# Kernel optimization log

Measured on AMD Instinct MI355X. Metric: run time of the kernel, lower is better.

Reference implementation:

```python
import jax, jax.numpy as jnp
import numpy as np

B, T, C = 16, 2048, 64  # n_embd = 64


def setup_inputs() -> dict:
    key = jax.random.key(0)
    ks = jax.random.split(key, 4)
    scale = 1.0 / np.sqrt(C)
    x = jax.random.normal(ks[0], (B, T, C), dtype=jnp.float32)
    Wk = jax.random.normal(ks[1], (C, C), dtype=jnp.float32) * scale
    Wq = jax.random.normal(ks[2], (C, C), dtype=jnp.float32) * scale
    Wv = jax.random.normal(ks[3], (C, C), dtype=jnp.float32) * scale
    bk = jnp.zeros((C,), dtype=jnp.float32)
    bq = jnp.zeros((C,), dtype=jnp.float32)
    bv = jnp.zeros((C,), dtype=jnp.float32)
    return {"x": x, "Wk": Wk, "bk": bk, "Wq": Wq, "bq": bq, "Wv": Wv, "bv": bv}


def reference(x, Wk, bk, Wq, bq, Wv, bv):
    # Faithful to source: wei = q @ k^T * C**0.5 (MULTIPLY, as in original code),
    # softmax over last axis, no causal mask (tril is built but unused), dropout=0.
    _, _, c = x.shape
    k = jnp.einsum('btc,cd->btd', x, Wk) + bk
    q = jnp.einsum('btc,cd->btd', x, Wq) + bq
    v = jnp.einsum('btc,cd->btd', x, Wv) + bv
    wei = jnp.einsum('btd,bsd->bts', q, k) * (c ** 0.5)  # [B,T,T]
    wei = jax.nn.softmax(wei, axis=-1)
    out = jnp.einsum('bts,bsd->btd', wei, v)  # [B,T,C]
    return out
```

## Files before the change

### kernel.cpp

```cpp
#include <hip/hip_runtime.h>
#include <hip/hip_bf16.h>
#include <stdint.h>

#define NBATCH 16
#define NT 2048
#define NC 64
#define QT 128
#define KT 128
#define SC_LOG2E 11.5415603f

typedef __bf16 bf16x8 __attribute__((ext_vector_type(8)));
typedef float f32x4 __attribute__((ext_vector_type(4)));
typedef float f32x16 __attribute__((ext_vector_type(16)));

#define Z16 {0.f,0.f,0.f,0.f,0.f,0.f,0.f,0.f,0.f,0.f,0.f,0.f,0.f,0.f,0.f,0.f}

extern "C" __device__ float __ocml_exp2_f32(float);

static __device__ __forceinline__ unsigned short f2bf(float f) {
  __bf16 h = (__bf16)f;
  union { __bf16 h; unsigned short u; } a; a.h = h; return a.u;
}
static __device__ __forceinline__ float bf2f(unsigned short h) {
  union { uint32_t u; float f; } a; a.u = ((uint32_t)h) << 16;
  return a.f;
}
static __device__ __forceinline__ float fasu(uint32_t u) {
  union { uint32_t u; float f; } a; a.u = u; return a.f;
}
static __device__ __forceinline__ uint32_t uasf(float f) {
  union { float f; uint32_t u; } a; a.f = f; return a.u;
}

#define GLD_LDS16(gsrc, ldst)                                                  \
  __builtin_amdgcn_global_load_lds(                                            \
      (const __attribute__((address_space(1))) void*)(gsrc),                   \
      (__attribute__((address_space(3))) void*)(ldst), 16, 0, 0)

__global__ __launch_bounds__(256, 2) void prep_w(
    const float* __restrict__ Wk, const float* __restrict__ Wq,
    const float* __restrict__ Wv,
    unsigned short* __restrict__ wt_hi, unsigned short* __restrict__ wt_lo)
{
  __shared__ unsigned short hbuf[64][66];
  __shared__ unsigned short lbuf[64][66];
  const int m = (int)blockIdx.x;
  const float* Wm = (m == 0) ? Wk : (m == 1 ? Wq : Wv);
  const int tid = (int)threadIdx.x;
  for (int idx = tid; idx < 1024; idx += 256) {
    int c = idx >> 4, o4 = (idx & 15) * 4;
    float4 v = *(const float4*)(Wm + c * 64 + o4);
    float vals[4] = {v.x, v.y, v.z, v.w};
#pragma unroll
    for (int j = 0; j < 4; ++j) {
      unsigned short h = f2bf(vals[j]);
      hbuf[o4 + j][c] = h;
      lbuf[o4 + j][c] = f2bf(vals[j] - bf2f(h));
    }
  }
  __syncthreads();
  for (int idx = tid; idx < 1024; idx += 256) {
    int o = idx >> 4, c0 = (idx & 15) * 4;
    ushort4 hv, lv;
    hv.x = hbuf[o][c0]; hv.y = hbuf[o][c0 + 1];
    hv.z = hbuf[o][c0 + 2]; hv.w = hbuf[o][c0 + 3];
    lv.x = lbuf[o][c0]; lv.y = lbuf[o][c0 + 1];
    lv.z = lbuf[o][c0 + 2]; lv.w = lbuf[o][c0 + 3];
    *(ushort4*)(wt_hi + (size_t)(m * 64 + o) * 64 + c0) = hv;
    *(ushort4*)(wt_lo + (size_t)(m * 64 + o) * 64 + c0) = lv;
  }
}

__global__ __launch_bounds__(256, 2) void proj_kernel(
    const float* __restrict__ x,
    const unsigned short* __restrict__ wt_hi, const unsigned short* __restrict__ wt_lo,
    const float* __restrict__ bk, const float* __restrict__ bq, const float* __restrict__ bv,
    unsigned short* __restrict__ khi, unsigned short* __restrict__ klo,
    unsigned short* __restrict__ qhi, unsigned short* __restrict__ qlo,
    unsigned short* __restrict__ vt)
{
  __shared__ __align__(16) char smem[65536];
  const int XH = 0, XL = 8192, WTH = 16384, WTL = 40960, VTB = 0;
  const int tid = (int)threadIdx.x;
  const int l = tid & 63, w = tid >> 6;
  const int lr = l & 15, lg = l >> 4;
  const int blk = (int)blockIdx.x;
  const int rowbase = blk * 64;
  const int bb = blk >> 5;

  float4 xv[4];
#pragma unroll
  for (int j = 0; j < 4; ++j) {
    int c = tid + j * 256;
    int row = c >> 4, d0 = (c & 15) * 4;
    xv[j] = *(const float4*)(x + (size_t)(rowbase + row) * NC + d0);
  }
#pragma unroll
  for (int ch4 = 0; ch4 < 6; ++ch4) {
    int ch = ch4 * 4 + w;
    int d = ch * 1024 + l * 16;
    int swk = d ^ (((d >> 7) & 7) << 4);
    GLD_LDS16((const char*)wt_hi + swk, smem + WTH + ch * 1024);
    GLD_LDS16((const char*)wt_lo + swk, smem + WTL + ch * 1024);
  }
#pragma unroll
  for (int j = 0; j < 4; ++j) {
    int c = tid + j * 256;
    int row = c >> 4, d0 = (c & 15) * 4;
    unsigned short h0 = f2bf(xv[j].x), h1 = f2bf(xv[j].y), h2 = f2bf(xv[j].z), h3 = f2bf(xv[j].w);
    unsigned short m0 = f2bf(xv[j].x - bf2f(h0)), m1 = f2bf(xv[j].y - bf2f(h1));
    unsigned short m2 = f2bf(xv[j].z - bf2f(h2)), m3 = f2bf(xv[j].w - bf2f(h3));
    uint2 ph, pl;
    ph.x = (uint32_t)h0 | ((uint32_t)h1 << 16); ph.y = (uint32_t)h2 | ((uint32_t)h3 << 16);
    pl.x = (uint32_t)m0 | ((uint32_t)m1 << 16); pl.y = (uint32_t)m2 | ((uint32_t)m3 << 16);
    int byteoff = (row * 128 + d0 * 2) ^ ((row & 7) << 4);
    *(uint2*)(smem + XH + byteoff) = ph;
    *(uint2*)(smem + XL + byteoff) = pl;
  }
  __syncthreads();

  bf16x8 xh[2], xl[2];
  {
    int row = w * 16 + lr;
#pragma unroll
    for (int dc = 0; dc < 2; ++dc) {
      int byteoff = (row * 128 + (dc * 32 + lg * 8) * 2) ^ ((row & 7) << 4);
      xh[dc] = *(const bf16x8*)(smem + XH + byteoff);
      xl[dc] = *(const bf16x8*)(smem + XL + byteoff);
    }
  }
  f32x4 acc[12];
#pragma unroll
  for (int nb = 0; nb < 12; ++nb) {
    f32x4 a = {0.f, 0.f, 0.f, 0.f};
    int og = nb * 16 + lr;
#pragma unroll
    for (int dc = 0; dc < 2; ++dc) {
      int byteoff = (og * 128 + (dc * 32 + lg * 8) * 2) ^ ((og & 7) << 4);
      bf16x8 bh = *(const bf16x8*)(smem + WTH + byteoff);
      bf16x8 bl = *(const bf16x8*)(smem + WTL + byteoff);
      a = __builtin_amdgcn_mfma_f32_16x16x32_bf16(bh, xh[dc], a, 0, 0, 0);
      a = __builtin_amdgcn_mfma_f32_16x16x32_bf16(bl, xh[dc], a, 0, 0, 0);
      a = __builtin_amdgcn_mfma_f32_16x16x32_bf16(bh, xl[dc], a, 0, 0, 0);
    }
    acc[nb] = a;
  }
  __syncthreads();

  const int tloc = w * 16 + lr;
  const size_t gt = (size_t)(rowbase + tloc);
#pragma unroll
  for (int nb = 0; nb < 12; ++nb) {
    int ogb = (nb & 3) * 16 + lg * 4;
    const float* bp = (nb < 4) ? bk : (nb < 8 ? bq : bv);
    float4 bias = *(const float4*)(bp + ogb);
    float v0 = acc[nb][0] + bias.x, v1 = acc[nb][1] + bias.y,
          v2 = acc[nb][2] + bias.z, v3 = acc[nb][3] + bias.w;
    if (nb < 8) {
      if (nb >= 4) { v0 *= SC_LOG2E; v1 *= SC_LOG2E; v2 *= SC_LOG2E; v3 *= SC_LOG2E; }
      ushort4 hv, lv;
      hv.x = f2bf(v0); lv.x = f2bf(v0 - bf2f(hv.x));
      hv.y = f2bf(v1); lv.y = f2bf(v1 - bf2f(hv.y));
      hv.z = f2bf(v2); lv.z = f2bf(v2 - bf2f(hv.z));
      hv.w = f2bf(v3); lv.w = f2bf(v3 - bf2f(hv.w));
      unsigned short* dH = (nb < 4) ? khi : qhi;
      unsigned short* dL = (nb < 4) ? klo : qlo;
      *(ushort4*)(dH + gt * 64 + ogb) = hv;
      *(ushort4*)(dL + gt * 64 + ogb) = lv;
    } else {
      float vs[4] = {v0, v1, v2, v3};
#pragma unroll
      for (int r = 0; r < 4; ++r) {
        int o = ogb + r;
        int byteoff = (o * 128 + tloc * 2) ^ ((o & 7) << 4);
        *(unsigned short*)(smem + VTB + byteoff) = f2bf(vs[r]);
      }
    }
  }
  __syncthreads();
  for (int cc = tid; cc < 512; cc += 256) {
    int o = cc >> 3, t0 = (cc & 7) * 8;
    int byteoff = (o * 128 + t0 * 2) ^ ((o & 7) << 4);
    uint4 v = *(const uint4*)(smem + VTB + byteoff);
    *(uint4*)(vt + ((size_t)bb * 64 + o) * NT + (size_t)(blk & 31) * 64 + t0) = v;
  }
}

__global__ __launch_bounds__(512, 2) void attn_kernel(
    const unsigned short* __restrict__ khi, const unsigned short* __restrict__ klo,
    const unsigned short* __restrict__ qhi, const unsigned short* __restrict__ qlo,
    const unsigned short* __restrict__ vt,
    float* __restrict__ out)
{
  __shared__ __align__(16) char smem[98304];
  const int BUF = 49152;
  const int MLB = 65536;
  const int tid = (int)threadIdx.x;
  const int l = tid & 63, w = tid >> 6;
  const int lq = l & 31;
  const bool hi = (l >= 32);
  const int hioff = hi ? 16 : 0;
  const int r = w & 3;
  const int cc = w >> 2;
  const int lb = ((int)(blockIdx.x & 7) << 5) | ((int)blockIdx.x >> 3);
  const int bb = lb >> 4;
  const int qt = lb & 15;

  const char* kh_base = (const char*)(khi + (size_t)bb * NT * 64);
  const char* kl_base = (const char*)(klo + (size_t)bb * NT * 64);
  const char* v_base  = (const char*)(vt + (size_t)bb * 64 * NT);

#define STAGE_TILE(bufp_, it_)                                                 \
  do {                                                                         \
    const char* kh_t = kh_base + (size_t)(it_) * 16384;                        \
    const char* kl_t = kl_base + (size_t)(it_) * 16384;                        \
    const char* v_tb = v_base + (size_t)(it_) * 256;                           \
    _Pragma("unroll")                                                          \
    for (int j = 0; j < 2; ++j) {                                              \
      int ch = 2 * w + j;                                                      \
      int d = ch * 1024 + l * 16;                                              \
      int swk = d ^ (((d >> 7) & 7) << 4);                                     \
      GLD_LDS16(kh_t + swk, (bufp_) + ch * 1024);                              \
      GLD_LDS16(kl_t + swk, (bufp_) + 16384 + ch * 1024);                      \
      int o = d >> 8;                                                          \
      int swv = (d ^ ((o & 7) << 4)) & 255;                                    \
      GLD_LDS16(v_tb + (size_t)o * 4096 + swv, (bufp_) + 32768 + ch * 1024);   \
    }                                                                          \
  } while (0)

  STAGE_TILE(smem, 0);
  bf16x8 Qh[4], Ql[4];
  {
    const char* qh_t = (const char*)qhi + ((size_t)bb * NT + (size_t)qt * QT) * 128;
    const char* ql_t = (const char*)qlo + ((size_t)bb * NT + (size_t)qt * QT) * 128;
    int qrow = r * 32 + lq;
#pragma unroll
    for (int dc = 0; dc < 4; ++dc) {
      Qh[dc] = *(const bf16x8*)(qh_t + qrow * 128 + dc * 32 + hioff);
      Ql[dc] = *(const bf16x8*)(ql_t + qrow * 128 + dc * 32 + hioff);
    }
  }
  asm volatile("s_waitcnt vmcnt(0)" ::: "memory");
  __builtin_amdgcn_s_barrier();
  asm volatile("" ::: "memory");

  f32x16 O0 = Z16, O1 = Z16;
  float mrun = -1e30f, lrun = 0.f;
  const int swr = (lq & 7) << 4;

  for (int it = 0; it < NT / KT; ++it) {
    char* cb = smem + (it & 1) * BUF;
    if (it + 1 < NT / KT) STAGE_TILE(smem + ((it + 1) & 1) * BUF, it + 1);

    f32x16 T1a = Z16, T2a = Z16, T3a = Z16;
    f32x16 T1b = Z16, T2b = Z16, T3b = Z16;
    __builtin_amdgcn_s_setprio(1);
    {
      int row0 = cc * 64 + lq;
      int row1 = row0 + 32;
#pragma unroll
      for (int dc = 0; dc < 4; ++dc) {
        int cchunk = (dc * 32 + hioff) ^ swr;
        bf16x8 Ah0 = *(const bf16x8*)(cb + row0 * 128 + cchunk);
        bf16x8 Al0 = *(const bf16x8*)(cb + 16384 + row0 * 128 + cchunk);
        bf16x8 Ah1 = *(const bf16x8*)(cb + row1 * 128 + cchunk);
        bf16x8 Al1 = *(const bf16x8*)(cb + 16384 + row1 * 128 + cchunk);
        T1a = __builtin_amdgcn_mfma_f32_32x32x16_bf16(Ah0, Qh[dc], T1a, 0, 0, 0);
        T1b = __builtin_amdgcn_mfma_f32_32x32x16_bf16(Ah1, Qh[dc], T1b, 0, 0, 0);
        T2a = __builtin_amdgcn_mfma_f32_32x32x16_bf16(Al0, Qh[dc], T2a, 0, 0, 0);
        T2b = __builtin_amdgcn_mfma_f32_32x32x16_bf16(Al1, Qh[dc], T2b, 0, 0, 0);
        T3a = __builtin_amdgcn_mfma_f32_32x32x16_bf16(Ah0, Ql[dc], T3a, 0, 0, 0);
        T3b = __builtin_amdgcn_mfma_f32_32x32x16_bf16(Ah1, Ql[dc], T3b, 0, 0, 0);
      }
    }
    __builtin_amdgcn_s_setprio(0);
    f32x16 S0 = (T1a + T2a) + T3a;
    f32x16 S1 = (T1b + T2b) + T3b;

    float m01 = fmaxf(S0[0], S0[1]),   m23 = fmaxf(S0[2], S0[3]);
    float m45 = fmaxf(S0[4], S0[5]),   m67 = fmaxf(S0[6], S0[7]);
    float m89 = fmaxf(S0[8], S0[9]),   mab = fmaxf(S0[10], S0[11]);
    float mcd = fmaxf(S0[12], S0[13]), mef = fmaxf(S0[14], S0[15]);
    float pmax = fmaxf(fmaxf(fmaxf(m01, m23), fmaxf(m45, m67)),
                       fmaxf(fmaxf(m89, mab), fmaxf(mcd, mef)));
    m01 = fmaxf(S1[0], S1[1]);   m23 = fmaxf(S1[2], S1[3]);
    m45 = fmaxf(S1[4], S1[5]);   m67 = fmaxf(S1[6], S1[7]);
    m89 = fmaxf(S1[8], S1[9]);   mab = fmaxf(S1[10], S1[11]);
    mcd = fmaxf(S1[12], S1[13]); mef = fmaxf(S1[14], S1[15]);
    pmax = fmaxf(pmax, fmaxf(fmaxf(fmaxf(m01, m23), fmaxf(m45, m67)),
                             fmaxf(fmaxf(m89, mab), fmaxf(mcd, mef))));
    {
      auto sw = __builtin_amdgcn_permlane32_swap(uasf(pmax), uasf(pmax), false, false);
      pmax = fmaxf(fasu(sw[0]), fasu(sw[1]));
    }
    if (__any(pmax > mrun + 11.55f)) {
      float mnew = fmaxf(mrun, pmax);
      float alpha = __ocml_exp2_f32(mrun - mnew);
      O0 *= alpha; O1 *= alpha; lrun *= alpha; mrun = mnew;
    }
    float p0[16], p1[16];
    float ts = 0.f;
#pragma unroll
    for (int i = 0; i < 16; ++i) { p0[i] = __ocml_exp2_f32(S0[i] - mrun); ts += p0[i]; }
#pragma unroll
    for (int i = 0; i < 16; ++i) { p1[i] = __ocml_exp2_f32(S1[i] - mrun); ts += p1[i]; }
    {
      auto sw = __builtin_amdgcn_permlane32_swap(uasf(ts), uasf(ts), false, false);
      ts = fasu(sw[0]) + fasu(sw[1]);
    }
    lrun += ts;

#define PV_CHUNK(kc_, PARR)                                                    \
    {                                                                          \
      const int b_ = 8 * ((kc_) & 1);                                          \
      uint32_t X0, X1, Y0, Y1;                                                 \
      asm("v_cvt_pk_bf16_f32 %0, %1, %2" : "=v"(X0) : "v"(PARR[b_+0]), "v"(PARR[b_+1])); \
      asm("v_cvt_pk_bf16_f32 %0, %1, %2" : "=v"(X1) : "v"(PARR[b_+2]), "v"(PARR[b_+3])); \
      asm("v_cvt_pk_bf16_f32 %0, %1, %2" : "=v"(Y0) : "v"(PARR[b_+4]), "v"(PARR[b_+5])); \
      asm("v_cvt_pk_bf16_f32 %0, %1, %2" : "=v"(Y1) : "v"(PARR[b_+6]), "v"(PARR[b_+7])); \
      auto sw0 = __builtin_amdgcn_permlane32_swap(X0, Y0, false, false);       \
      auto sw1 = __builtin_amdgcn_permlane32_swap(X1, Y1, false, false);       \
      union { uint32_t u[4]; bf16x8 v; } cvb;                                  \
      cvb.u[0] = sw0[0]; cvb.u[1] = sw1[0];                                    \
      cvb.u[2] = sw0[1]; cvb.u[3] = sw1[1];                                    \
      bf16x8 Bp = cvb.v;                                                       \
      int vcol = 128 * cc + 32 * (kc_) + hioff;                                \
      {                                                                        \
        bf16x8 Av = *(const bf16x8*)(cb + 32768 + lq * 256 + (vcol ^ swr));    \
        O0 = __builtin_amdgcn_mfma_f32_32x32x16_bf16(Av, Bp, O0, 0, 0, 0);     \
      }                                                                        \
      {                                                                        \
        bf16x8 Av = *(const bf16x8*)(cb + 32768 + (32 + lq) * 256 + (vcol ^ swr)); \
        O1 = __builtin_amdgcn_mfma_f32_32x32x16_bf16(Av, Bp, O1, 0, 0, 0);     \
      }                                                                        \
    }
    __builtin_amdgcn_s_setprio(1);
    PV_CHUNK(0, p0)
    PV_CHUNK(1, p0)
    PV_CHUNK(2, p1)
    PV_CHUNK(3, p1)
    __builtin_amdgcn_s_setprio(0);
#undef PV_CHUNK

    asm volatile("s_waitcnt vmcnt(0)" ::: "memory");
    __builtin_amdgcn_s_barrier();
    asm volatile("" ::: "memory");
    __builtin_amdgcn_sched_barrier(0);
  }

  const int lsw = (l & 7) << 4;
  if (cc == 1) {
    char* dd = smem + r * 8192 + l * 128;
#pragma unroll
    for (int g = 0; g < 4; ++g) {
      f32x4 t0, t1;
#pragma unroll
      for (int j = 0; j < 4; ++j) { t0[j] = O0[4*g+j]; t1[j] = O1[4*g+j]; }
      *(f32x4*)(dd + ((g * 16) ^ lsw)) = t0;
      *(f32x4*)(dd + ((64 + g * 16) ^ lsw)) = t1;
    }
    *(float*)(smem + MLB + r * 256 + lq * 8) = mrun;
    *(float*)(smem + MLB + r * 256 + lq * 8 + 4) = lrun;
  }
  __syncthreads();
  if (cc == 0) {
    const char* ds = smem + r * 8192 + l * 128;
    float m1 = *(const float*)(smem + MLB + r * 256 + lq * 8);
    float l1 = *(const float*)(smem + MLB + r * 256 + lq * 8 + 4);
    float M = fmaxf(mrun, m1);
    float a0 = __ocml_exp2_f32(mrun - M);
    float a1 = __ocml_exp2_f32(m1 - M);
    float Lt = lrun * a0 + l1 * a1;
    float inv = 1.0f / Lt;
    float f0 = a0 * inv, f1 = a1 * inv;
    float* orow = out + ((size_t)bb * NT + (size_t)qt * QT + r * 32 + lq) * 64;
#pragma unroll
    for (int g = 0; g < 4; ++g) {
      f32x4 o1a = *(const f32x4*)(ds + ((g * 16) ^ lsw));
      f32x4 o1b = *(const f32x4*)(ds + ((64 + g * 16) ^ lsw));
      int d0 = 8 * g + (hi ? 4 : 0);
      f32x4 s0, s1;
#pragma unroll
      for (int j = 0; j < 4; ++j) {
        s0[j] = O0[4*g+j] * f0 + o1a[j] * f1;
        s1[j] = O1[4*g+j] * f0 + o1b[j] * f1;
      }
      *(f32x4*)(orow + d0) = s0;
      *(f32x4*)(orow + d0 + 32) = s1;
    }
  }
#undef STAGE_TILE
}

extern "C" void kernel_launch(void* const* d_in, const int* in_sizes, int n_in,
                              void* d_out, int out_size, void* d_ws, size_t ws_size,
                              hipStream_t stream) {
  const float* x  = (const float*)d_in[0];
  const float* Wk = (const float*)d_in[1];
  const float* bk = (const float*)d_in[2];
  const float* Wq = (const float*)d_in[3];
  const float* bq = (const float*)d_in[4];
  const float* Wv = (const float*)d_in[5];
  const float* bv = (const float*)d_in[6];
  float* out = (float*)d_out;

  const size_t NE = (size_t)NBATCH * NT * 64;
  unsigned short* ws = (unsigned short*)d_ws;
  unsigned short* khi = ws;
  unsigned short* klo = ws + NE;
  unsigned short* qhi = ws + 2 * NE;
  unsigned short* qlo = ws + 3 * NE;
  unsigned short* vt  = ws + 4 * NE;
  unsigned short* wt_hi = ws + 5 * NE;
  unsigned short* wt_lo = wt_hi + 192 * 64;

  prep_w<<<dim3(3), dim3(256), 0, stream>>>(Wk, Wq, Wv, wt_hi, wt_lo);
  proj_kernel<<<dim3((NBATCH * NT) / 64), dim3(256), 0, stream>>>(
      x, wt_hi, wt_lo, bk, bq, bv, khi, klo, qhi, qlo, vt);
  attn_kernel<<<dim3(NBATCH * (NT / QT)), dim3(512), 0, stream>>>(
      khi, klo, qhi, qlo, vt, out);
}
```

Measured before the change: 74.75 us.

## Software-pipeline QK of next tile with softmax/PV of previous tile

Restructures the attention loop so that the QK^T MFMAs for tile i+1 are issued before the softmax and PV work for tile i, overlapping the exp/VALU work with the matrix engine. K is double-buffered and V triple-buffered in LDS, which raises the LDS allocation to 112KB. The three split-precision accumulators are also merged into a single accumulation chain, and the exp2 calls switch to the native (less accurate) variant. The larger LDS footprint may reduce occupancy below two blocks per CU, and the extra live score registers add register pressure.

New measurement: 65.41 us. 12.5% less time.

```diff
diff --git a/kernel.cpp b/kernel.cpp
--- a/kernel.cpp
+++ b/kernel.cpp
@@ -15,7 +15,8 @@
 
 #define Z16 {0.f,0.f,0.f,0.f,0.f,0.f,0.f,0.f,0.f,0.f,0.f,0.f,0.f,0.f,0.f,0.f}
 
-extern "C" __device__ float __ocml_exp2_f32(float);
+extern "C" __device__ float __ocml_native_exp2_f32(float);
+#define EXP2F(x) __ocml_native_exp2_f32(x)
 
 static __device__ __forceinline__ unsigned short f2bf(float f) {
   __bf16 h = (__bf16)f;
@@ -192,9 +193,10 @@
     const unsigned short* __restrict__ vt,
     float* __restrict__ out)
 {
-  __shared__ __align__(16) char smem[98304];
-  const int BUF = 49152;
-  const int MLB = 65536;
+  __shared__ __align__(16) char smem[114688];
+  const int KB_A = 0, KB_B = 32768;
+  const int VB_0 = 65536, VB_1 = 81920, VB_2 = 98304;
+  const int MLB = 40960;
   const int tid = (int)threadIdx.x;
   const int l = tid & 63, w = tid >> 6;
   const int lq = l & 31;
@@ -210,7 +212,7 @@
   const char* kl_base = (const char*)(klo + (size_t)bb * NT * 64);
   const char* v_base  = (const char*)(vt + (size_t)bb * 64 * NT);
 
-#define STAGE_TILE(bufp_, it_)                                                 \
+#define STAGE_TILE(kb_, vb_, it_)                                              \
   do {                                                                         \
     const char* kh_t = kh_base + (size_t)(it_) * 16384;                        \
     const char* kl_t = kl_base + (size_t)(it_) * 16384;                        \
@@ -220,15 +222,16 @@
       int ch = 2 * w + j;                                                      \
       int d = ch * 1024 + l * 16;                                              \
       int swk = d ^ (((d >> 7) & 7) << 4);                                     \
-      GLD_LDS16(kh_t + swk, (bufp_) + ch * 1024);                              \
-      GLD_LDS16(kl_t + swk, (bufp_) + 16384 + ch * 1024);                      \
+      GLD_LDS16(kh_t + swk, smem + (kb_) + ch * 1024);                         \
+      GLD_LDS16(kl_t + swk, smem + (kb_) + 16384 + ch * 1024);                 \
       int o = d >> 8;                                                          \
       int swv = (d ^ ((o & 7) << 4)) & 255;                                    \
-      GLD_LDS16(v_tb + (size_t)o * 4096 + swv, (bufp_) + 32768 + ch * 1024);   \
+      GLD_LDS16(v_tb + (size_t)o * 4096 + swv, smem + (vb_) + ch * 1024);      \
     }                                                                          \
   } while (0)
 
-  STAGE_TILE(smem, 0);
+  STAGE_TILE(KB_A, VB_0, 0);
+  STAGE_TILE(KB_B, VB_1, 1);
   bf16x8 Qh[4], Ql[4];
   {
     const char* qh_t = (const char*)qhi + ((size_t)bb * NT + (size_t)qt * QT) * 128;
@@ -248,105 +251,125 @@
   float mrun = -1e30f, lrun = 0.f;
   const int swr = (lq & 7) << 4;
 
-  for (int it = 0; it < NT / KT; ++it) {
-    char* cb = smem + (it & 1) * BUF;
-    if (it + 1 < NT / KT) STAGE_TILE(smem + ((it + 1) & 1) * BUF, it + 1);
-
-    f32x16 T1a = Z16, T2a = Z16, T3a = Z16;
-    f32x16 T1b = Z16, T2b = Z16, T3b = Z16;
-    __builtin_amdgcn_s_setprio(1);
-    {
-      int row0 = cc * 64 + lq;
-      int row1 = row0 + 32;
-#pragma unroll
-      for (int dc = 0; dc < 4; ++dc) {
-        int cchunk = (dc * 32 + hioff) ^ swr;
-        bf16x8 Ah0 = *(const bf16x8*)(cb + row0 * 128 + cchunk);
-        bf16x8 Al0 = *(const bf16x8*)(cb + 16384 + row0 * 128 + cchunk);
-        bf16x8 Ah1 = *(const bf16x8*)(cb + row1 * 128 + cchunk);
-        bf16x8 Al1 = *(const bf16x8*)(cb + 16384 + row1 * 128 + cchunk);
-        T1a = __builtin_amdgcn_mfma_f32_32x32x16_bf16(Ah0, Qh[dc], T1a, 0, 0, 0);
-        T1b = __builtin_amdgcn_mfma_f32_32x32x16_bf16(Ah1, Qh[dc], T1b, 0, 0, 0);
-        T2a = __builtin_amdgcn_mfma_f32_32x32x16_bf16(Al0, Qh[dc], T2a, 0, 0, 0);
-        T2b = __builtin_amdgcn_mfma_f32_32x32x16_bf16(Al1, Qh[dc], T2b, 0, 0, 0);
-        T3a = __builtin_amdgcn_mfma_f32_32x32x16_bf16(Ah0, Ql[dc], T3a, 0, 0, 0);
-        T3b = __builtin_amdgcn_mfma_f32_32x32x16_bf16(Ah1, Ql[dc], T3b, 0, 0, 0);
-      }
-    }
-    __builtin_amdgcn_s_setprio(0);
-    f32x16 S0 = (T1a + T2a) + T3a;
-    f32x16 S1 = (T1b + T2b) + T3b;
-
-    float m01 = fmaxf(S0[0], S0[1]),   m23 = fmaxf(S0[2], S0[3]);
-    float m45 = fmaxf(S0[4], S0[5]),   m67 = fmaxf(S0[6], S0[7]);
-    float m89 = fmaxf(S0[8], S0[9]),   mab = fmaxf(S0[10], S0[11]);
-    float mcd = fmaxf(S0[12], S0[13]), mef = fmaxf(S0[14], S0[15]);
-    float pmax = fmaxf(fmaxf(fmaxf(m01, m23), fmaxf(m45, m67)),
-                       fmaxf(fmaxf(m89, mab), fmaxf(mcd, mef)));
-    m01 = fmaxf(S1[0], S1[1]);   m23 = fmaxf(S1[2], S1[3]);
-    m45 = fmaxf(S1[4], S1[5]);   m67 = fmaxf(S1[6], S1[7]);
-    m89 = fmaxf(S1[8], S1[9]);   mab = fmaxf(S1[10], S1[11]);
-    mcd = fmaxf(S1[12], S1[13]); mef = fmaxf(S1[14], S1[15]);
-    pmax = fmaxf(pmax, fmaxf(fmaxf(fmaxf(m01, m23), fmaxf(m45, m67)),
-                             fmaxf(fmaxf(m89, mab), fmaxf(mcd, mef))));
-    {
-      auto sw = __builtin_amdgcn_permlane32_swap(uasf(pmax), uasf(pmax), false, false);
-      pmax = fmaxf(fasu(sw[0]), fasu(sw[1]));
-    }
-    if (__any(pmax > mrun + 11.55f)) {
-      float mnew = fmaxf(mrun, pmax);
-      float alpha = __ocml_exp2_f32(mrun - mnew);
-      O0 *= alpha; O1 *= alpha; lrun *= alpha; mrun = mnew;
-    }
-    float p0[16], p1[16];
-    float ts = 0.f;
-#pragma unroll
-    for (int i = 0; i < 16; ++i) { p0[i] = __ocml_exp2_f32(S0[i] - mrun); ts += p0[i]; }
-#pragma unroll
-    for (int i = 0; i < 16; ++i) { p1[i] = __ocml_exp2_f32(S1[i] - mrun); ts += p1[i]; }
-    {
-      auto sw = __builtin_amdgcn_permlane32_swap(uasf(ts), uasf(ts), false, false);
-      ts = fasu(sw[0]) + fasu(sw[1]);
-    }
-    lrun += ts;
-
-#define PV_CHUNK(kc_, PARR)                                                    \
+#define QK_TILE(kb_, SC0_, SC1_)                                               \
+  {                                                                            \
+    int row0_ = cc * 64 + lq;                                                  \
+    int row1_ = row0_ + 32;                                                    \
+    __builtin_amdgcn_s_setprio(1);                                             \
+    _Pragma("unroll")                                                          \
+    for (int dc = 0; dc < 4; ++dc) {                                           \
+      int cchunk_ = (dc * 32 + hioff) ^ swr;                                   \
+      bf16x8 Ah0_ = *(const bf16x8*)(smem + (kb_) + row0_ * 128 + cchunk_);    \
+      bf16x8 Al0_ = *(const bf16x8*)(smem + (kb_) + 16384 + row0_ * 128 + cchunk_); \
+      bf16x8 Ah1_ = *(const bf16x8*)(smem + (kb_) + row1_ * 128 + cchunk_);    \
+      bf16x8 Al1_ = *(const bf16x8*)(smem + (kb_) + 16384 + row1_ * 128 + cchunk_); \
+      SC0_ = __builtin_amdgcn_mfma_f32_32x32x16_bf16(Ah0_, Qh[dc], SC0_, 0, 0, 0); \
+      SC1_ = __builtin_amdgcn_mfma_f32_32x32x16_bf16(Ah1_, Qh[dc], SC1_, 0, 0, 0); \
+      SC0_ = __builtin_amdgcn_mfma_f32_32x32x16_bf16(Al0_, Qh[dc], SC0_, 0, 0, 0); \
+      SC1_ = __builtin_amdgcn_mfma_f32_32x32x16_bf16(Al1_, Qh[dc], SC1_, 0, 0, 0); \
+      SC0_ = __builtin_amdgcn_mfma_f32_32x32x16_bf16(Ah0_, Ql[dc], SC0_, 0, 0, 0); \
+      SC1_ = __builtin_amdgcn_mfma_f32_32x32x16_bf16(Ah1_, Ql[dc], SC1_, 0, 0, 0); \
+    }                                                                          \
+    __builtin_amdgcn_s_setprio(0);                                             \
+  }
+
+#define SMPV(SP0_, SP1_, vb_)                                                  \
+  {                                                                            \
+    float a01 = fmaxf(SP0_[0], SP0_[1]),   a23 = fmaxf(SP0_[2], SP0_[3]);      \
+    float a45 = fmaxf(SP0_[4], SP0_[5]),   a67 = fmaxf(SP0_[6], SP0_[7]);      \
+    float a89 = fmaxf(SP0_[8], SP0_[9]),   aab = fmaxf(SP0_[10], SP0_[11]);    \
+    float acd = fmaxf(SP0_[12], SP0_[13]), aef = fmaxf(SP0_[14], SP0_[15]);    \
+    float pmax = fmaxf(fmaxf(fmaxf(a01, a23), fmaxf(a45, a67)),                \
+                       fmaxf(fmaxf(a89, aab), fmaxf(acd, aef)));               \
+    a01 = fmaxf(SP1_[0], SP1_[1]);   a23 = fmaxf(SP1_[2], SP1_[3]);            \
+    a45 = fmaxf(SP1_[4], SP1_[5]);   a67 = fmaxf(SP1_[6], SP1_[7]);            \
+    a89 = fmaxf(SP1_[8], SP1_[9]);   aab = fmaxf(SP1_[10], SP1_[11]);          \
+    acd = fmaxf(SP1_[12], SP1_[13]); aef = fmaxf(SP1_[14], SP1_[15]);          \
+    pmax = fmaxf(pmax, fmaxf(fmaxf(fmaxf(a01, a23), fmaxf(a45, a67)),          \
+                             fmaxf(fmaxf(a89, aab), fmaxf(acd, aef))));        \
     {                                                                          \
-      const int b_ = 8 * ((kc_) & 1);                                          \
+      auto sw_ = __builtin_amdgcn_permlane32_swap(uasf(pmax), uasf(pmax), false, false); \
+      pmax = fmaxf(fasu(sw_[0]), fasu(sw_[1]));                                \
+    }                                                                          \
+    if (__any(pmax > mrun + 11.55f)) {                                         \
+      float mnew = fmaxf(mrun, pmax);                                          \
+      float alpha = EXP2F(mrun - mnew);                                        \
+      O0 *= alpha; O1 *= alpha; lrun *= alpha; mrun = mnew;                    \
+    }                                                                          \
+    float p0[16], p1[16];                                                      \
+    float ts = 0.f;                                                            \
+    _Pragma("unroll")                                                          \
+    for (int i = 0; i < 16; ++i) { p0[i] = EXP2F(SP0_[i] - mrun); ts += p0[i]; } \
+    _Pragma("unroll")                                                          \
+    for (int i = 0; i < 16; ++i) { p1[i] = EXP2F(SP1_[i] - mrun); ts += p1[i]; } \
+    {                                                                          \
+      auto sw_ = __builtin_amdgcn_permlane32_swap(uasf(ts), uasf(ts), false, false); \
+      ts = fasu(sw_[0]) + fasu(sw_[1]);                                        \
+    }                                                                          \
+    lrun += ts;                                                                \
+    __builtin_amdgcn_s_setprio(1);                                             \
+    _Pragma("unroll")                                                          \
+    for (int kc = 0; kc < 4; ++kc) {                                           \
+      const int b_ = 8 * (kc & 1);                                             \
       uint32_t X0, X1, Y0, Y1;                                                 \
-      asm("v_cvt_pk_bf16_f32 %0, %1, %2" : "=v"(X0) : "v"(PARR[b_+0]), "v"(PARR[b_+1])); \
-      asm("v_cvt_pk_bf16_f32 %0, %1, %2" : "=v"(X1) : "v"(PARR[b_+2]), "v"(PARR[b_+3])); \
-      asm("v_cvt_pk_bf16_f32 %0, %1, %2" : "=v"(Y0) : "v"(PARR[b_+4]), "v"(PARR[b_+5])); \
-      asm("v_cvt_pk_bf16_f32 %0, %1, %2" : "=v"(Y1) : "v"(PARR[b_+6]), "v"(PARR[b_+7])); \
-      auto sw0 = __builtin_amdgcn_permlane32_swap(X0, Y0, false, false);       \
-      auto sw1 = __builtin_amdgcn_permlane32_swap(X1, Y1, false, false);       \
-      union { uint32_t u[4]; bf16x8 v; } cvb;                                  \
-      cvb.u[0] = sw0[0]; cvb.u[1] = sw1[0];                                    \
-      cvb.u[2] = sw0[1]; cvb.u[3] = sw1[1];                                    \
-      bf16x8 Bp = cvb.v;                                                       \
-      int vcol = 128 * cc + 32 * (kc_) + hioff;                                \
-      {                                                                        \
-        bf16x8 Av = *(const bf16x8*)(cb + 32768 + lq * 256 + (vcol ^ swr));    \
-        O0 = __builtin_amdgcn_mfma_f32_32x32x16_bf16(Av, Bp, O0, 0, 0, 0);     \
+      if (kc < 2) {                                                            \
+        asm("v_cvt_pk_bf16_f32 %0, %1, %2" : "=v"(X0) : "v"(p0[b_+0]), "v"(p0[b_+1])); \
+        asm("v_cvt_pk_bf16_f32 %0, %1, %2" : "=v"(X1) : "v"(p0[b_+2]), "v"(p0[b_+3])); \
+        asm("v_cvt_pk_bf16_f32 %0, %1, %2" : "=v"(Y0) : "v"(p0[b_+4]), "v"(p0[b_+5])); \
+        asm("v_cvt_pk_bf16_f32 %0, %1, %2" : "=v"(Y1) : "v"(p0[b_+6]), "v"(p0[b_+7])); \
+      } else {                                                                 \
+        asm("v_cvt_pk_bf16_f32 %0, %1, %2" : "=v"(X0) : "v"(p1[b_+0]), "v"(p1[b_+1])); \
+        asm("v_cvt_pk_bf16_f32 %0, %1, %2" : "=v"(X1) : "v"(p1[b_+2]), "v"(p1[b_+3])); \
+        asm("v_cvt_pk_bf16_f32 %0, %1, %2" : "=v"(Y0) : "v"(p1[b_+4]), "v"(p1[b_+5])); \
+        asm("v_cvt_pk_bf16_f32 %0, %1, %2" : "=v"(Y1) : "v"(p1[b_+6]), "v"(p1[b_+7])); \
       }                                                                        \
-      {                                                                        \
-        bf16x8 Av = *(const bf16x8*)(cb + 32768 + (32 + lq) * 256 + (vcol ^ swr)); \
-        O1 = __builtin_amdgcn_mfma_f32_32x32x16_bf16(Av, Bp, O1, 0, 0, 0);     \
-      }                                                                        \
-    }
-    __builtin_amdgcn_s_setprio(1);
-    PV_CHUNK(0, p0)
-    PV_CHUNK(1, p0)
-    PV_CHUNK(2, p1)
-    PV_CHUNK(3, p1)
-    __builtin_amdgcn_s_setprio(0);
-#undef PV_CHUNK
-
-    asm volatile("s_waitcnt vmcnt(0)" ::: "memory");
-    __builtin_amdgcn_s_barrier();
-    asm volatile("" ::: "memory");
-    __builtin_amdgcn_sched_barrier(0);
-  }
+      auto sw0_ = __builtin_amdgcn_permlane32_swap(X0, Y0, false, false);      \
+      auto sw1_ = __builtin_amdgcn_permlane32_swap(X1, Y1, false, false);      \
+      union { uint32_t u[4]; bf16x8 v; } cvb_;                                 \
+      cvb_.u[0] = sw0_[0]; cvb_.u[1] = sw1_[0];                                \
+      cvb_.u[2] = sw0_[1]; cvb_.u[3] = sw1_[1];                                \
+      int vcol_ = 128 * cc + 32 * kc + hioff;                                  \
+      bf16x8 Av0_ = *(const bf16x8*)(smem + (vb_) + lq * 256 + (vcol_ ^ swr)); \
+      bf16x8 Av1_ = *(const bf16x8*)(smem + (vb_) + (32 + lq) * 256 + (vcol_ ^ swr)); \
+      O0 = __builtin_amdgcn_mfma_f32_32x32x16_bf16(Av0_, cvb_.v, O0, 0, 0, 0); \
+      O1 = __builtin_amdgcn_mfma_f32_32x32x16_bf16(Av1_, cvb_.v, O1, 0, 0, 0); \
+    }                                                                          \
+    __builtin_amdgcn_s_setprio(0);                                             \
+  }
+
+  f32x16 SA0 = Z16, SA1 = Z16, SB0 = Z16, SB1 = Z16;
+  QK_TILE(KB_A, SA0, SA1);
+  asm volatile("s_waitcnt lgkmcnt(0)" ::: "memory");
+  __builtin_amdgcn_s_barrier();
+  asm volatile("" ::: "memory");
+
+  int kbC = KB_B, kbN = KB_A;
+  int vbP = VB_0, vbC = VB_1, vbN = VB_2;
+
+#define BODY(i_, SP0_, SP1_, SC0_, SC1_, STG_)                                 \
+  {                                                                            \
+    if (STG_) STAGE_TILE(kbN, vbN, (i_) + 1);                                  \
+    SC0_ = Z16; SC1_ = Z16;                                                    \
+    QK_TILE(kbC, SC0_, SC1_);                                                  \
+    SMPV(SP0_, SP1_, vbP);                                                     \
+    asm volatile("s_waitcnt vmcnt(0)" ::: "memory");                           \
+    __builtin_amdgcn_s_barrier();                                              \
+    asm volatile("" ::: "memory");                                             \
+    __builtin_amdgcn_sched_barrier(0);                                         \
+  }
+#define ROT()                                                                  \
+  { int t_ = vbP; vbP = vbC; vbC = vbN; vbN = t_;                              \
+    t_ = kbC; kbC = kbN; kbN = t_; }
+
+#pragma unroll 1
+  for (int ib = 0; ib < 7; ++ib) {
+    BODY(2 * ib + 1, SA0, SA1, SB0, SB1, 1)
+    ROT()
+    BODY(2 * ib + 2, SB0, SB1, SA0, SA1, 1)
+    ROT()
+  }
+  BODY(15, SA0, SA1, SB0, SB1, 0)
+  SMPV(SB0, SB1, vbC);
 
   const int lsw = (l & 7) << 4;
   if (cc == 1) {
@@ -368,8 +391,8 @@
     float m1 = *(const float*)(smem + MLB + r * 256 + lq * 8);
     float l1 = *(const float*)(smem + MLB + r * 256 + lq * 8 + 4);
     float M = fmaxf(mrun, m1);
-    float a0 = __ocml_exp2_f32(mrun - M);
-    float a1 = __ocml_exp2_f32(m1 - M);
+    float a0 = EXP2F(mrun - M);
+    float a1 = EXP2F(m1 - M);
     float Lt = lrun * a0 + l1 * a1;
     float inv = 1.0f / Lt;
     float f0 = a0 * inv, f1 = a1 * inv;
@@ -389,6 +412,10 @@
       *(f32x4*)(orow + d0 + 32) = s1;
     }
   }
+#undef BODY
+#undef ROT
+#undef SMPV
+#undef QK_TILE
 #undef STAGE_TILE
 }
 
```
